# Kernel optimization log

Measured on AMD Instinct MI355X. Metric: run time of the kernel, lower is better.

The kernel has to match this reference:

```python
import jax, jax.numpy as jnp
import numpy as np

TAU = 0.001
TEMPERATURE = 0.1


def setup_inputs() -> dict:
    key = jax.random.key(0)
    k1, k2 = jax.random.split(key)
    B, H, N, L = 2, 8, 256, 64
    X = jax.random.normal(k1, (B, H, N, L), dtype=jnp.float32)
    Y = jax.random.normal(k2, (B, H, N, L), dtype=jnp.float32)
    return {"X": X, "Y": Y}


def _softsort_p2(scores):
    # scores: [B,H,N,L] -> s: [B,H,L,N]
    s = jnp.transpose(scores, (0, 1, 3, 2))
    srt = -jnp.sort(-s, axis=-1)  # descending sort along N
    # pairwise squared diff: rows = sorted values, cols = original values -> [B,H,L,N,N]
    pd = -((s[..., None, :] - srt[..., :, None]) ** 2) / TAU
    return jax.nn.softmax(pd, axis=-1)


def reference(X, Y):
    # Soft permutation matrices: [B,H,L,N,N]
    Pu = _softsort_p2(X)
    Pv = _softsort_p2(Y)
    # Gamma = Pu^T @ Pv  (contract over sorted-row index i)
    Gamma = jnp.einsum('bhlij,bhlik->bhljk', Pu, Pv)
    # cdist(X, Y, p=2) over last dim L -> [B,H,N,N]
    x2 = jnp.sum(X * X, axis=-1)            # [B,H,N]
    y2 = jnp.sum(Y * Y, axis=-1)            # [B,H,N]
    xy = jnp.einsum('bhnl,bhml->bhnm', X, Y)
    cost = jnp.sqrt(jnp.maximum(x2[..., :, None] + y2[..., None, :] - 2.0 * xy, 1e-12))
    # swds[b,h,l] = sum_{j,k} cost[b,h,j,k] * Gamma[b,h,l,j,k]
    swds = jnp.einsum('bhjk,bhljk->bhl', cost, Gamma)
    # exp(-T*(swds - min)) / sum == softmax(-T * swds) over L
    weights = jax.nn.softmax(-TEMPERATURE * swds, axis=-1)  # [B,H,L]
    # weighted sum over L -> [B,H,N,N]
    return jnp.einsum('bhljk,bhl->bhjk', Gamma, weights)
```

## Files before the change

### kernel.cpp

```cpp
#include <hip/hip_runtime.h>
#include <math.h>

#define INV_TAU 1000.0f
#define TEMP    0.1f
#define CEXP    -1442.6950408889634f
#define SQRTC   37.98283767f


typedef __attribute__((ext_vector_type(8))) _Float16 half8;
typedef __attribute__((ext_vector_type(8))) short short8;
typedef __attribute__((ext_vector_type(4))) float f32x4;
typedef __attribute__((ext_vector_type(2))) unsigned int u32x2;

__device__ __forceinline__ float fexp2(float x) { return __builtin_amdgcn_exp2f(x); }

__device__ __forceinline__ half8 ldsh8(const unsigned short* p) {
  return __builtin_bit_cast(half8, *(const short8*)p);
}

__device__ __forceinline__ unsigned bf16r(float f) {
  unsigned u = __float_as_uint(f);
  return (u + 0x7FFFu + ((u >> 16) & 1u)) >> 16;
}

__device__ __forceinline__ int tswz(int row, int g) {
  return row * 32 + (((g + (row >> 1)) & 3) << 3);
}

__global__ __launch_bounds__(256) void prep_kernel(const float* __restrict__ X,
                                                   const float* __restrict__ Y,
                                                   float* __restrict__ cost,
                                                   float* __restrict__ nssu, float* __restrict__ lziu,
                                                   float* __restrict__ nssv, float* __restrict__ lziv) {
  __shared__ __align__(16) float smem[256];
  const int tid = threadIdx.x;
  if (blockIdx.x < 1024) {
    const int jq = blockIdx.x & 63, bh = blockIdx.x >> 6;
    const int j0 = jq * 4;
    smem[tid] = X[((size_t)bh*256 + j0 + (tid >> 6))*64 + (tid & 63)];
    __syncthreads();
    const float4* yp = (const float4*)(Y + ((size_t)bh*256 + tid)*64);
    float dot[4] = {0.f,0.f,0.f,0.f}, x2[4] = {0.f,0.f,0.f,0.f}, y2 = 0.f;
#pragma unroll
    for (int t = 0; t < 16; ++t) {
      float4 yv = yp[t];
      y2 += yv.x*yv.x + yv.y*yv.y + yv.z*yv.z + yv.w*yv.w;
#pragma unroll
      for (int r = 0; r < 4; ++r) {
        float4 xv = ((const float4*)(smem + r*64))[t];
        dot[r] += xv.x*yv.x + xv.y*yv.y + xv.z*yv.z + xv.w*yv.w;
        x2[r]  += xv.x*xv.x + xv.y*xv.y + xv.z*xv.z + xv.w*xv.w;
      }
    }
#pragma unroll
    for (int r = 0; r < 4; ++r) {
      float c = x2[r] + y2 - 2.f*dot[r];
      cost[((size_t)bh*256 + j0 + r)*256 + tid] = sqrtf(fmaxf(c, 1e-12f));
    }
  } else {
    const int idx = blockIdx.x - 1024;
    const int l = idx & 63, bh = (idx >> 6) & 15, uv = idx >> 10;
    const float* S = uv ? Y : X;
    float* so = uv ? nssv : nssu;
    float* zo = uv ? lziv : lziu;
    float v = S[((size_t)bh*256 + tid)*64 + l];
#pragma unroll
    for (int k = 2; k <= 256; k <<= 1) {
#pragma unroll
      for (int j = k >> 1; j > 0; j >>= 1) {
        float o;
        if (j >= 64) {
          smem[tid] = v; __syncthreads();
          o = smem[tid ^ j]; __syncthreads();
        } else {
          o = __shfl_xor(v, j, 64);
        }
        const bool up    = ((tid & k) == 0);
        const bool lower = ((tid & j) == 0);
        float mn = fminf(v, o), mx = fmaxf(v, o);
        v = (up == lower) ? mn : mx;
      }
    }
    smem[tid] = v; __syncthreads();
    const int jc = 255 - tid;
    const float sv = smem[jc];
    const int lo = jc > 48 ? jc - 48 : 0;
    const int hi = jc < 207 ? jc + 48 : 255;
    float z = 0.f;
    for (int jj = lo; jj <= hi; ++jj) { float d = smem[jj] - sv; z += fexp2(d*d*CEXP); }
    const int base = (bh*64 + l)*256 + tid;
    so[base] = -SQRTC * sv; zo[base] = -__log2f(z);
  }
}

__device__ __forceinline__ void stage_slab(int t, int ib, float usc, float vsc,
                                           const float* __restrict__ nssU, const float* __restrict__ lzU,
                                           const float* __restrict__ nssV, const float* __restrict__ lzV,
                                           unsigned short* __restrict__ EU,
                                           unsigned short* __restrict__ EV) {
  {
    const int r = t & 127, g = t >> 7;
    const int i0 = ib + (g << 3);
    float e[8];
#pragma unroll
    for (int ii = 0; ii < 8; ++ii) {
      float d = usc + nssU[i0 + ii];
      e[ii] = fexp2(fmaf(-d, d, lzU[i0 + ii]));
    }
    uint4 w;
    w.x = __builtin_bit_cast(unsigned, __builtin_amdgcn_cvt_pkrtz(e[0], e[1]));
    w.y = __builtin_bit_cast(unsigned, __builtin_amdgcn_cvt_pkrtz(e[2], e[3]));
    w.z = __builtin_bit_cast(unsigned, __builtin_amdgcn_cvt_pkrtz(e[4], e[5]));
    w.w = __builtin_bit_cast(unsigned, __builtin_amdgcn_cvt_pkrtz(e[6], e[7]));
    *(uint4*)&EU[tswz(r, g)] = w;
  }
  {
    const int r = t & 255;
    const int gp = (t >> 8) << 1;
#pragma unroll
    for (int gg = 0; gg < 2; ++gg) {
      const int i0 = ib + ((gp + gg) << 3);
      float e[8];
#pragma unroll
      for (int ii = 0; ii < 8; ++ii) {
        float d = vsc + nssV[i0 + ii];
        e[ii] = fexp2(fmaf(-d, d, lzV[i0 + ii]));
      }
      uint4 w;
      w.x = __builtin_bit_cast(unsigned, __builtin_amdgcn_cvt_pkrtz(e[0], e[1]));
      w.y = __builtin_bit_cast(unsigned, __builtin_amdgcn_cvt_pkrtz(e[2], e[3]));
      w.z = __builtin_bit_cast(unsigned, __builtin_amdgcn_cvt_pkrtz(e[4], e[5]));
      w.w = __builtin_bit_cast(unsigned, __builtin_amdgcn_cvt_pkrtz(e[6], e[7]));
      *(uint4*)&EV[tswz(r, gp + gg)] = w;
    }
  }
}

__global__ __launch_bounds__(512, 4) void pass1_kernel(
    const float* __restrict__ X, const float* __restrict__ Y,
    const float* __restrict__ cost,
    const float* __restrict__ nssu, const float* __restrict__ lziu,
    const float* __restrict__ nssv, const float* __restrict__ lziv,
    float* __restrict__ parts, u32x2* __restrict__ gamma) {
  const int sb = blockIdx.x, l = blockIdx.y, bh = blockIdx.z;
  const int j0 = sb * 128;
  const int tid = threadIdx.x, wave = tid >> 6, lane = tid & 63;
  const int wj = (wave & 1) * 64, wk = (wave >> 1) * 64;
  const int m = lane & 15, q = lane >> 4;
  const int inner = m*32 + (((q + (m >> 1)) & 3) << 3);

  __shared__ float nssU[256], lzU[256], nssV[256], lzV[256];
  __shared__ __align__(16) unsigned short EU0[128*32], EU1[128*32];
  __shared__ __align__(16) unsigned short EV0[256*32], EV1[256*32];
  __shared__ float red[8];

  const int lb = (bh*64 + l)*256;
  const float usc = SQRTC * X[((size_t)bh*256 + j0 + (tid & 127))*64 + l];
  const float vsc = SQRTC * Y[((size_t)bh*256 + (tid & 255))*64 + l];
  if (tid < 256) { nssU[tid] = nssu[lb + tid]; lzU[tid] = lziu[lb + tid]; }
  else { const int t2 = tid - 256; nssV[t2] = nssv[lb + t2]; lzV[t2] = lziv[lb + t2]; }

  f32x4 acc[16];
#pragma unroll
  for (int t = 0; t < 16; ++t) acc[t] = (f32x4){0.f, 0.f, 0.f, 0.f};

  __syncthreads();
  stage_slab(tid, 0, usc, vsc, nssU, lzU, nssV, lzV, EU0, EV0);
  __syncthreads();
#pragma unroll 1
  for (int s = 0; s < 8; ++s) {
    const unsigned short* EUc = (s & 1) ? EU1 : EU0;
    const unsigned short* EVc = (s & 1) ? EV1 : EV0;
    unsigned short* EUn = (s & 1) ? EU0 : EU1;
    unsigned short* EVn = (s & 1) ? EV0 : EV1;
    half8 A[4], B[4];
#pragma unroll
    for (int mt = 0; mt < 4; ++mt) A[mt] = ldsh8(&EUc[(wj + mt*16)*32 + inner]);
#pragma unroll
    for (int nt = 0; nt < 4; ++nt) B[nt] = ldsh8(&EVc[(wk + nt*16)*32 + inner]);
    if (s < 7)
      stage_slab(tid, (s+1)*32, usc, vsc, nssU, lzU, nssV, lzV, EUn, EVn);
#pragma unroll
    for (int mt = 0; mt < 4; ++mt)
#pragma unroll
      for (int nt = 0; nt < 4; ++nt)
        acc[mt*4+nt] = __builtin_amdgcn_mfma_f32_16x16x32_f16(A[mt], B[nt], acc[mt*4+nt], 0, 0, 0);
    __syncthreads();
  }

  const float* cb = cost + (size_t)bh * 65536;
  const int gbase = ((bh*2 + sb)*8 + wave) * 16;
  float part = 0.f;
#pragma unroll
  for (int mt = 0; mt < 4; ++mt) {
#pragma unroll
    for (int nt = 0; nt < 4; ++nt) {
      const int col  = wk + nt*16 + m;
      const int rowb = j0 + wj + mt*16 + q*4;
      f32x4 a = acc[mt*4 + nt];
      part += a.x*cb[(size_t)(rowb+0)*256 + col] + a.y*cb[(size_t)(rowb+1)*256 + col]
            + a.z*cb[(size_t)(rowb+2)*256 + col] + a.w*cb[(size_t)(rowb+3)*256 + col];
      u32x2 pk;
      pk.x = bf16r(a.x) | (bf16r(a.y) << 16);
      pk.y = bf16r(a.z) | (bf16r(a.w) << 16);
      __builtin_nontemporal_store(pk, &gamma[((size_t)(gbase + mt*4 + nt)*64 + l)*64 + lane]);
    }
  }
#pragma unroll
  for (int o = 32; o > 0; o >>= 1) part += __shfl_down(part, o, 64);
  if (lane == 0) red[wave] = part;
  __syncthreads();
  if (tid == 0) {
    float s8 = red[0]+red[1]+red[2]+red[3]+red[4]+red[5]+red[6]+red[7];
    parts[sb*1024 + bh*64 + l] = s8;
  }
}

__global__ __launch_bounds__(256) void wsum_kernel(const u32x2* __restrict__ g,
                                                   const float* __restrict__ parts,
                                                   float* __restrict__ out) {
  const int wv = threadIdx.x >> 6, lane = threadIdx.x & 63;
  const int bh = blockIdx.x >> 6;
  __shared__ float w[64];
  if (wv == 0) {
    float s = parts[bh*64 + lane] + parts[1024 + bh*64 + lane];
    float v = -TEMP * s * 1.4426950408889634f;
    float mx = v;
#pragma unroll
    for (int o = 32; o > 0; o >>= 1) mx = fmaxf(mx, __shfl_xor(mx, o, 64));
    float e = fexp2(v - mx);
    float ssum = e;
#pragma unroll
    for (int o = 32; o > 0; o >>= 1) ssum += __shfl_xor(ssum, o, 64);
    w[lane] = e / ssum;
  }
  __syncthreads();
  const int group = blockIdx.x * 4 + wv;
  const u32x2* gp = g + (size_t)group*4096 + lane;
  float4 acc = {0.f, 0.f, 0.f, 0.f};
#pragma unroll 8
  for (int l = 0; l < 64; ++l) {
    u32x2 pk = __builtin_nontemporal_load(gp + l*64);
    float wl = w[l];
    acc.x += wl * __uint_as_float(pk.x << 16);
    acc.y += wl * __uint_as_float(pk.x & 0xFFFF0000u);
    acc.z += wl * __uint_as_float(pk.y << 16);
    acc.w += wl * __uint_as_float(pk.y & 0xFFFF0000u);
  }
  const int frag = group & 15;
  const int idx  = group >> 4;
  const int wave = idx & 7, sbb = (idx >> 3) & 1;
  const int mt = frag >> 2, nt = frag & 3;
  const int m = lane & 15, q = lane >> 4;
  const int row = sbb*128 + (wave & 1)*64 + mt*16 + q*4;
  const int col = (wave >> 1)*64 + nt*16 + m;
  float* ob = out + ((size_t)bh*256 + row)*256 + col;
  __builtin_nontemporal_store(acc.x, &ob[0]);
  __builtin_nontemporal_store(acc.y, &ob[256]);
  __builtin_nontemporal_store(acc.z, &ob[512]);
  __builtin_nontemporal_store(acc.w, &ob[768]);
}

extern "C" void kernel_launch(void* const* d_in, const int* in_sizes, int n_in,
                              void* d_out, int out_size, void* d_ws, size_t ws_size,
                              hipStream_t stream) {
  (void)in_sizes; (void)n_in; (void)out_size; (void)ws_size;
  const float* X = (const float*)d_in[0];
  const float* Y = (const float*)d_in[1];
  float* out = (float*)d_out;
  float* ws  = (float*)d_ws;
  float* cost  = ws;
  float* nssu  = ws   + 1048576;
  float* lziu  = nssu + 262144;
  float* nssv  = lziu + 262144;
  float* lziv  = nssv + 262144;
  float* parts = lziv + 262144;
  u32x2* gamma = (u32x2*)(parts + 2048);

  prep_kernel <<<dim3(3072),      256, 0, stream>>>(X, Y, cost, nssu, lziu, nssv, lziv);
  pass1_kernel<<<dim3(2, 64, 16), 512, 0, stream>>>(X, Y, cost, nssu, lziu, nssv, lziv,
                                                    parts, gamma);
  wsum_kernel <<<dim3(1024),      256, 0, stream>>>(gamma, parts, out);
}
```

Baseline: 163.5 us.

## Merge row-split pass1 blocks into one 1024-thread block per (bh,l)

Result: slower. 170.2 us (+4.1%).

```diff
diff --git a/kernel.cpp b/kernel.cpp
--- a/kernel.cpp
+++ b/kernel.cpp
@@ -93,79 +93,65 @@
   }
 }
 
-__device__ __forceinline__ void stage_slab(int t, int ib, float usc, float vsc,
+__device__ __forceinline__ uint4 oct_exp(const float* __restrict__ nss,
+                                         const float* __restrict__ lz, float sc) {
+  float e[8];
+#pragma unroll
+  for (int ii = 0; ii < 8; ++ii) {
+    float d = sc + nss[ii];
+    e[ii] = fexp2(fmaf(-d, d, lz[ii]));
+  }
+  uint4 w;
+  w.x = __builtin_bit_cast(unsigned, __builtin_amdgcn_cvt_pkrtz(e[0], e[1]));
+  w.y = __builtin_bit_cast(unsigned, __builtin_amdgcn_cvt_pkrtz(e[2], e[3]));
+  w.z = __builtin_bit_cast(unsigned, __builtin_amdgcn_cvt_pkrtz(e[4], e[5]));
+  w.w = __builtin_bit_cast(unsigned, __builtin_amdgcn_cvt_pkrtz(e[6], e[7]));
+  return w;
+}
+
+__device__ __forceinline__ void stage_slab(int r, int g, int ib, float usc, float vsc,
                                            const float* __restrict__ nssU, const float* __restrict__ lzU,
                                            const float* __restrict__ nssV, const float* __restrict__ lzV,
                                            unsigned short* __restrict__ EU,
                                            unsigned short* __restrict__ EV) {
-  {
-    const int r = t & 127, g = t >> 7;
-    const int i0 = ib + (g << 3);
-    float e[8];
-#pragma unroll
-    for (int ii = 0; ii < 8; ++ii) {
-      float d = usc + nssU[i0 + ii];
-      e[ii] = fexp2(fmaf(-d, d, lzU[i0 + ii]));
-    }
-    uint4 w;
-    w.x = __builtin_bit_cast(unsigned, __builtin_amdgcn_cvt_pkrtz(e[0], e[1]));
-    w.y = __builtin_bit_cast(unsigned, __builtin_amdgcn_cvt_pkrtz(e[2], e[3]));
-    w.z = __builtin_bit_cast(unsigned, __builtin_amdgcn_cvt_pkrtz(e[4], e[5]));
-    w.w = __builtin_bit_cast(unsigned, __builtin_amdgcn_cvt_pkrtz(e[6], e[7]));
-    *(uint4*)&EU[tswz(r, g)] = w;
-  }
-  {
-    const int r = t & 255;
-    const int gp = (t >> 8) << 1;
-#pragma unroll
-    for (int gg = 0; gg < 2; ++gg) {
-      const int i0 = ib + ((gp + gg) << 3);
-      float e[8];
-#pragma unroll
-      for (int ii = 0; ii < 8; ++ii) {
-        float d = vsc + nssV[i0 + ii];
-        e[ii] = fexp2(fmaf(-d, d, lzV[i0 + ii]));
-      }
-      uint4 w;
-      w.x = __builtin_bit_cast(unsigned, __builtin_amdgcn_cvt_pkrtz(e[0], e[1]));
-      w.y = __builtin_bit_cast(unsigned, __builtin_amdgcn_cvt_pkrtz(e[2], e[3]));
-      w.z = __builtin_bit_cast(unsigned, __builtin_amdgcn_cvt_pkrtz(e[4], e[5]));
-      w.w = __builtin_bit_cast(unsigned, __builtin_amdgcn_cvt_pkrtz(e[6], e[7]));
-      *(uint4*)&EV[tswz(r, gp + gg)] = w;
-    }
-  }
-}
-
-__global__ __launch_bounds__(512, 4) void pass1_kernel(
+  const int i0  = ib + (g << 3);
+  const int off = tswz(r, g);
+  *(uint4*)&EU[off] = oct_exp(nssU + i0, lzU + i0, usc);
+  *(uint4*)&EV[off] = oct_exp(nssV + i0, lzV + i0, vsc);
+}
+
+__global__ __launch_bounds__(1024) void pass1_kernel(
     const float* __restrict__ X, const float* __restrict__ Y,
     const float* __restrict__ cost,
     const float* __restrict__ nssu, const float* __restrict__ lziu,
     const float* __restrict__ nssv, const float* __restrict__ lziv,
     float* __restrict__ parts, u32x2* __restrict__ gamma) {
-  const int sb = blockIdx.x, l = blockIdx.y, bh = blockIdx.z;
-  const int j0 = sb * 128;
+  const int l = blockIdx.x, bh = blockIdx.y;
   const int tid = threadIdx.x, wave = tid >> 6, lane = tid & 63;
-  const int wj = (wave & 1) * 64, wk = (wave >> 1) * 64;
+  const int wj = (wave & 3) * 64, wk = (wave >> 2) * 64;
   const int m = lane & 15, q = lane >> 4;
   const int inner = m*32 + (((q + (m >> 1)) & 3) << 3);
 
-  __shared__ float nssU[256], lzU[256], nssV[256], lzV[256];
-  __shared__ __align__(16) unsigned short EU0[128*32], EU1[128*32];
+  __shared__ __align__(16) float nssU[256], lzU[256], nssV[256], lzV[256];
+  __shared__ __align__(16) unsigned short EU0[256*32], EU1[256*32];
   __shared__ __align__(16) unsigned short EV0[256*32], EV1[256*32];
-  __shared__ float red[8];
+  __shared__ float red[16];
 
   const int lb = (bh*64 + l)*256;
-  const float usc = SQRTC * X[((size_t)bh*256 + j0 + (tid & 127))*64 + l];
-  const float vsc = SQRTC * Y[((size_t)bh*256 + (tid & 255))*64 + l];
-  if (tid < 256) { nssU[tid] = nssu[lb + tid]; lzU[tid] = lziu[lb + tid]; }
-  else { const int t2 = tid - 256; nssV[t2] = nssv[lb + t2]; lzV[t2] = lziv[lb + t2]; }
+  const int r = tid & 255, g = tid >> 8;
+  const float usc = SQRTC * X[((size_t)bh*256 + r)*64 + l];
+  const float vsc = SQRTC * Y[((size_t)bh*256 + r)*64 + l];
+  if (g == 0)      nssU[r] = nssu[lb + r];
+  else if (g == 1) lzU[r]  = lziu[lb + r];
+  else if (g == 2) nssV[r] = nssv[lb + r];
+  else             lzV[r]  = lziv[lb + r];
 
   f32x4 acc[16];
 #pragma unroll
   for (int t = 0; t < 16; ++t) acc[t] = (f32x4){0.f, 0.f, 0.f, 0.f};
 
   __syncthreads();
-  stage_slab(tid, 0, usc, vsc, nssU, lzU, nssV, lzV, EU0, EV0);
+  stage_slab(r, g, 0, usc, vsc, nssU, lzU, nssV, lzV, EU0, EV0);
   __syncthreads();
 #pragma unroll 1
   for (int s = 0; s < 8; ++s) {
@@ -179,7 +165,7 @@
 #pragma unroll
     for (int nt = 0; nt < 4; ++nt) B[nt] = ldsh8(&EVc[(wk + nt*16)*32 + inner]);
     if (s < 7)
-      stage_slab(tid, (s+1)*32, usc, vsc, nssU, lzU, nssV, lzV, EUn, EVn);
+      stage_slab(r, g, (s+1)*32, usc, vsc, nssU, lzU, nssV, lzV, EUn, EVn);
 #pragma unroll
     for (int mt = 0; mt < 4; ++mt)
 #pragma unroll
@@ -189,21 +175,21 @@
   }
 
   const float* cb = cost + (size_t)bh * 65536;
-  const int gbase = ((bh*2 + sb)*8 + wave) * 16;
+  const int gbase = (bh*16 + wave) * 16;
   float part = 0.f;
 #pragma unroll
   for (int mt = 0; mt < 4; ++mt) {
 #pragma unroll
     for (int nt = 0; nt < 4; ++nt) {
       const int col  = wk + nt*16 + m;
-      const int rowb = j0 + wj + mt*16 + q*4;
+      const int rowb = wj + mt*16 + q*4;
       f32x4 a = acc[mt*4 + nt];
       part += a.x*cb[(size_t)(rowb+0)*256 + col] + a.y*cb[(size_t)(rowb+1)*256 + col]
             + a.z*cb[(size_t)(rowb+2)*256 + col] + a.w*cb[(size_t)(rowb+3)*256 + col];
       u32x2 pk;
       pk.x = bf16r(a.x) | (bf16r(a.y) << 16);
       pk.y = bf16r(a.z) | (bf16r(a.w) << 16);
-      __builtin_nontemporal_store(pk, &gamma[((size_t)(gbase + mt*4 + nt)*64 + l)*64 + lane]);
+      gamma[((size_t)(gbase + mt*4 + nt)*64 + l)*64 + lane] = pk;
     }
   }
 #pragma unroll
@@ -211,8 +197,10 @@
   if (lane == 0) red[wave] = part;
   __syncthreads();
   if (tid == 0) {
-    float s8 = red[0]+red[1]+red[2]+red[3]+red[4]+red[5]+red[6]+red[7];
-    parts[sb*1024 + bh*64 + l] = s8;
+    float s16 = 0.f;
+#pragma unroll
+    for (int i = 0; i < 16; ++i) s16 += red[i];
+    parts[bh*64 + l] = s16;
   }
 }
 
@@ -223,7 +211,7 @@
   const int bh = blockIdx.x >> 6;
   __shared__ float w[64];
   if (wv == 0) {
-    float s = parts[bh*64 + lane] + parts[1024 + bh*64 + lane];
+    float s = parts[bh*64 + lane];
     float v = -TEMP * s * 1.4426950408889634f;
     float mx = v;
 #pragma unroll
@@ -240,7 +228,7 @@
   float4 acc = {0.f, 0.f, 0.f, 0.f};
 #pragma unroll 8
   for (int l = 0; l < 64; ++l) {
-    u32x2 pk = __builtin_nontemporal_load(gp + l*64);
+    u32x2 pk = gp[l*64];
     float wl = w[l];
     acc.x += wl * __uint_as_float(pk.x << 16);
     acc.y += wl * __uint_as_float(pk.x & 0xFFFF0000u);
@@ -248,17 +236,16 @@
     acc.w += wl * __uint_as_float(pk.y & 0xFFFF0000u);
   }
   const int frag = group & 15;
-  const int idx  = group >> 4;
-  const int wave = idx & 7, sbb = (idx >> 3) & 1;
+  const int gw   = (group >> 4) & 15;
   const int mt = frag >> 2, nt = frag & 3;
   const int m = lane & 15, q = lane >> 4;
-  const int row = sbb*128 + (wave & 1)*64 + mt*16 + q*4;
-  const int col = (wave >> 1)*64 + nt*16 + m;
+  const int row = (gw & 3)*64 + mt*16 + q*4;
+  const int col = (gw >> 2)*64 + nt*16 + m;
   float* ob = out + ((size_t)bh*256 + row)*256 + col;
-  __builtin_nontemporal_store(acc.x, &ob[0]);
-  __builtin_nontemporal_store(acc.y, &ob[256]);
-  __builtin_nontemporal_store(acc.z, &ob[512]);
-  __builtin_nontemporal_store(acc.w, &ob[768]);
+  ob[0]   = acc.x;
+  ob[256] = acc.y;
+  ob[512] = acc.z;
+  ob[768] = acc.w;
 }
 
 extern "C" void kernel_launch(void* const* d_in, const int* in_sizes, int n_in,
@@ -277,8 +264,8 @@
   float* parts = lziv + 262144;
   u32x2* gamma = (u32x2*)(parts + 2048);
 
-  prep_kernel <<<dim3(3072),      256, 0, stream>>>(X, Y, cost, nssu, lziu, nssv, lziv);
-  pass1_kernel<<<dim3(2, 64, 16), 512, 0, stream>>>(X, Y, cost, nssu, lziu, nssv, lziv,
-                                                    parts, gamma);
-  wsum_kernel <<<dim3(1024),      256, 0, stream>>>(gamma, parts, out);
-}
+  prep_kernel <<<dim3(3072),    256,  0, stream>>>(X, Y, cost, nssu, lziu, nssv, lziv);
+  pass1_kernel<<<dim3(64, 16), 1024,  0, stream>>>(X, Y, cost, nssu, lziu, nssv, lziv,
+                                                   parts, gamma);
+  wsum_kernel <<<dim3(1024),    256,  0, stream>>>(gamma, parts, out);
+}
```
